# Optimization experiments

Hardware: AMD Instinct MI355X
Metric: run time of the kernel (lower is better)

The kernel has to match this reference:

```python
import jax, jax.numpy as jnp
import numpy as np

GRID, RC, RD, FEAT, HID, PE = 300, 48, 16, 27, 128, 2
B, S = 4096, 128


def _grid_sample(img, grid):
    # img: (G,C,H,W); grid: (G,B,S,2) with (x=width, y=height) in [-1,1]
    # bilinear, align_corners=True (matches torch F.grid_sample defaults used here)
    G, C, H, W = img.shape
    x = (grid[..., 0] + 1.0) * 0.5 * (W - 1)  # (G,B,S)
    y = (grid[..., 1] + 1.0) * 0.5 * (H - 1)
    x0f, y0f = jnp.floor(x), jnp.floor(y)
    x0 = jnp.clip(x0f, 0, W - 1).astype(jnp.int32)
    y0 = jnp.clip(y0f, 0, H - 1).astype(jnp.int32)
    x1 = jnp.clip(x0 + 1, 0, W - 1)
    y1 = jnp.clip(y0 + 1, 0, H - 1)
    wx = (x - x0f)[:, None]  # (G,1,B,S)
    wy = (y - y0f)[:, None]

    def gather(im, yi, xi):  # im (C,H,W), yi/xi (B,S) -> (C,B,S)
        return im[:, yi, xi]

    g = jax.vmap(gather)
    v00 = g(img, y0, x0)
    v01 = g(img, y0, x1)
    v10 = g(img, y1, x0)
    v11 = g(img, y1, x1)
    return (v00 * (1 - wy) * (1 - wx) + v01 * (1 - wy) * wx
            + v10 * wy * (1 - wx) + v11 * wy * wx)  # (G,C,B,S)


def _vm(vectors, matrices, pos):
    # pos: (B,S,3) -> (B,S,3*R)
    b, s = pos.shape[0], pos.shape[1]
    mat_coord = jnp.stack([jnp.stack([pos[..., (i + 1) % 3], pos[..., (i + 2) % 3]], -1)
                           for i in range(3)], 0)  # (3,B,S,2)
    zero = jnp.zeros_like(pos[..., 0])
    vec_coord = jnp.stack([jnp.stack([pos[..., i], zero], -1) for i in range(3)], 0)
    m = _grid_sample(matrices, mat_coord)  # (3,R,B,S)
    v = _grid_sample(vectors, vec_coord)   # (3,R,B,S)
    return (m * v).transpose(2, 3, 0, 1).reshape(b, s, -1)


_COEFFS = (2.0 ** np.linspace(0.0, PE - 1, PE)) * np.pi  # [pi, 2pi]


def _pe(x):
    parts = []
    for c in _COEFFS:
        parts.append(jnp.sin(c * x))
        parts.append(jnp.cos(c * x))
    return jnp.concatenate(parts, -1)


def setup_inputs() -> dict:
    key = jax.random.key(0)
    ks = jax.random.split(key, 12)
    x = jax.random.uniform(ks[0], (B, S, 6), dtype=jnp.float32) * 2.0 - 1.0
    vmc_vec = jax.random.normal(ks[1], (3, RC, GRID, 1), dtype=jnp.float32) * 0.1
    vmc_mat = jax.random.normal(ks[2], (3, RC, GRID, GRID), dtype=jnp.float32) * 0.1
    vmd_vec = jax.random.normal(ks[3], (3, RD, GRID, 1), dtype=jnp.float32) * 0.1
    vmd_mat = jax.random.normal(ks[4], (3, RD, GRID, GRID), dtype=jnp.float32) * 0.1
    feat_w = jax.random.normal(ks[5], (FEAT, 3 * RC), dtype=jnp.float32) / np.sqrt(3 * RC)
    din = (1 + 2 * PE) * (3 + FEAT)  # 150
    w1 = jax.random.normal(ks[6], (HID, din), dtype=jnp.float32) / np.sqrt(din)
    b1 = jnp.zeros((HID,), jnp.float32)
    w2 = jax.random.normal(ks[7], (HID, HID), dtype=jnp.float32) / np.sqrt(HID)
    b2 = jnp.zeros((HID,), jnp.float32)
    w3 = jax.random.normal(ks[8], (3, HID), dtype=jnp.float32) / np.sqrt(HID)
    b3 = jnp.zeros((3,), jnp.float32)
    return {"x": x, "vmc_vec": vmc_vec, "vmc_mat": vmc_mat, "vmd_vec": vmd_vec,
            "vmd_mat": vmd_mat, "feat_w": feat_w, "w1": w1, "b1": b1,
            "w2": w2, "b2": b2, "w3": w3, "b3": b3}


def reference(x, vmc_vec, vmc_mat, vmd_vec, vmd_mat, feat_w, w1, b1, w2, b2, w3, b3):
    pos = x[..., :3]
    dirn = x[..., 3:]
    feature = jnp.einsum('bsk,fk->bsf', _vm(vmc_vec, vmc_mat, pos), feat_w)  # (B,S,27)
    mlp_in = jnp.concatenate([feature, dirn, _pe(feature), _pe(dirn)], -1)  # (B,S,150)
    h = jax.nn.relu(jnp.einsum('bsi,hi->bsh', mlp_in, w1) + b1)
    h = jax.nn.relu(jnp.einsum('bsi,hi->bsh', h, w2) + b2)
    color = jax.nn.sigmoid(jnp.einsum('bsi,oi->bso', h, w3) + b3)  # (B,S,3)
    density = jax.nn.relu(jnp.sum(_vm(vmd_vec, vmd_mat, pos), -1, keepdims=True))
    return jnp.concatenate([color, density], -1)  # (B,S,4)
```

## Files before the change

### kernel.cpp

```cpp
#include <hip/hip_runtime.h>
#include <stdint.h>

typedef unsigned int u32;
typedef _Float16 f16;
typedef __attribute__((ext_vector_type(8))) _Float16 f16x8;
typedef __attribute__((ext_vector_type(4))) float f32x4;
typedef __attribute__((ext_vector_type(2))) float f32x2;

#define XMS 168
#define HS  136

#define WOFF_WEFF 0u
#define WOFF_W1SW 10240u
#define WOFF_W2SW 51200u
#define WOFF_W3SW 83968u
#define WOFF_VD   88064u
#define WOFF_TM   131072u
#define WS_NEED   17411072u

#define TBL_SCALE 64.0f
#define TBL_INV   (1.0f/64.0f)

__global__ void prep_k(const float* __restrict__ feat_w,
                       const float* __restrict__ vmc_vec,
                       const float* __restrict__ vmd_vec,
                       const float* __restrict__ w1,
                       const float* __restrict__ w2,
                       const float* __restrict__ w3,
                       f16* __restrict__ Weff, f16* __restrict__ W1sw,
                       f16* __restrict__ W2sw, f16* __restrict__ W3sw,
                       float* __restrict__ vd)
{
  const int N_WEFF = 5120, N_W1 = 20480, N_W2 = 16384, N_W3 = 2048, N_VD = 48;
  const int total = N_WEFF + N_W1 + N_W2 + N_W3 + N_VD;
  for (int t = blockIdx.x*blockDim.x + threadIdx.x; t < total; t += gridDim.x*blockDim.x){
    if (t < N_WEFF){
      int kb = t >> 10, n = (t >> 5) & 31, kk = t & 31, k = kb*32 + kk;
      float v = 0.f;
      if (n < 27 && k < 144)
        v = feat_w[n*144 + k] * 0.5f*(vmc_vec[k*300+149] + vmc_vec[k*300+150]) * TBL_INV;
      Weff[t] = (f16)v;
    } else if (t < N_WEFF + N_W1){
      int u = t - N_WEFF;
      int kb = u >> 12, n = (u >> 5) & 127, kk = u & 31, k = kb*32 + kk;
      W1sw[u] = (f16)((k < 150) ? w1[n*150 + k] : 0.f);
    } else if (t < N_WEFF + N_W1 + N_W2){
      int u = t - N_WEFF - N_W1;
      int kb = u >> 12, n = (u >> 5) & 127, kk = u & 31, k = kb*32 + kk;
      W2sw[u] = (f16)w2[n*128 + k];
    } else if (t < N_WEFF + N_W1 + N_W2 + N_W3){
      int u = t - N_WEFF - N_W1 - N_W2;
      int kb = u >> 9, n = (u >> 5) & 15, kk = u & 31, k = kb*32 + kk;
      W3sw[u] = (f16)((n < 3) ? w3[n*128 + k] : 0.f);
    } else {
      int k = t - N_WEFF - N_W1 - N_W2 - N_W3;
      vd[k] = 0.5f*(vmd_vec[k*300+149] + vmd_vec[k*300+150]) * TBL_INV;
    }
  }
}

__global__ void pack_feat_k(const float* __restrict__ src, u32* __restrict__ dst)
{
  __shared__ float tile[48*304];
  int i = blockIdx.x / 300, y = blockIdx.x % 300;
  const float* sp = src + (size_t)i*48*90000 + (size_t)y*300;
  for (int t = threadIdx.x; t < 48*300; t += 256){
    int r = t / 300, x = t - r*300;
    tile[r*304 + x] = sp[(size_t)r*90000 + x] * TBL_SCALE;
  }
  __syncthreads();
  u32* dp = dst + (size_t)(i*300 + y)*300*16;
  for (int t = threadIdx.x; t < 300*12; t += 256){
    int x = t / 12, cg = t - x*12;
    int c = cg*4;
    u32 v = __builtin_amdgcn_cvt_pk_fp8_f32(tile[c*304+x],     tile[(c+1)*304+x], 0, false);
    v     = __builtin_amdgcn_cvt_pk_fp8_f32(tile[(c+2)*304+x], tile[(c+3)*304+x], v, true);
    dp[x*16 + cg] = v;
  }
}

__global__ void pack_dens_k(const float* __restrict__ src, u32* __restrict__ dst)
{
  __shared__ float tile[16*304];
  int i = blockIdx.x / 300, y = blockIdx.x % 300;
  const float* sp = src + (size_t)i*16*90000 + (size_t)y*300;
  for (int t = threadIdx.x; t < 16*300; t += 256){
    int r = t / 300, x = t - r*300;
    tile[r*304 + x] = sp[(size_t)r*90000 + x] * TBL_SCALE;
  }
  __syncthreads();
  u32* dp = dst + (size_t)(i*300 + y)*300*16;
  for (int t = threadIdx.x; t < 300*4; t += 256){
    int x = t / 4, cg = t - x*4;
    int c = cg*4;
    u32 v = __builtin_amdgcn_cvt_pk_fp8_f32(tile[c*304+x],     tile[(c+1)*304+x], 0, false);
    v     = __builtin_amdgcn_cvt_pk_fp8_f32(tile[(c+2)*304+x], tile[(c+3)*304+x], v, true);
    dp[x*16 + 12 + cg] = v;
  }
}

__device__ __forceinline__ void decode16(uint4 q, float* o){
  f32x2 t;
  t = __builtin_amdgcn_cvt_pk_f32_fp8(q.x, false); o[0]=t[0];  o[1]=t[1];
  t = __builtin_amdgcn_cvt_pk_f32_fp8(q.x, true ); o[2]=t[0];  o[3]=t[1];
  t = __builtin_amdgcn_cvt_pk_f32_fp8(q.y, false); o[4]=t[0];  o[5]=t[1];
  t = __builtin_amdgcn_cvt_pk_f32_fp8(q.y, true ); o[6]=t[0];  o[7]=t[1];
  t = __builtin_amdgcn_cvt_pk_f32_fp8(q.z, false); o[8]=t[0];  o[9]=t[1];
  t = __builtin_amdgcn_cvt_pk_f32_fp8(q.z, true ); o[10]=t[0]; o[11]=t[1];
  t = __builtin_amdgcn_cvt_pk_f32_fp8(q.w, false); o[12]=t[0]; o[13]=t[1];
  t = __builtin_amdgcn_cvt_pk_f32_fp8(q.w, true ); o[14]=t[0]; o[15]=t[1];
}

__global__ __launch_bounds__(256, 4)
void main_k(const float* __restrict__ xin,
            const f16* __restrict__ WeffSw, const f16* __restrict__ W1sw,
            const f16* __restrict__ W2sw, const f16* __restrict__ W3sw,
            const float* __restrict__ vd,
            const uint4* __restrict__ Tm,
            const float* __restrict__ b1v, const float* __restrict__ b2v,
            const float* __restrict__ b3v, float* __restrict__ out)
{
  __shared__ __align__(16) f16 buf[64*XMS];
  __shared__ __align__(16) f16 bufH[64*HS];
  __shared__ float dLds[192];

  const int tid = threadIdx.x;
  const int l = tid & 63;
  const int w = tid >> 6;
  const size_t nidx = (size_t)blockIdx.x*64 + l;

  const float* xp = xin + nidx*6;
  float p0 = xp[0], p1 = xp[1], p2 = xp[2];

  float dd0=0.f, dd1=0.f, dd2=0.f;
  if (l < 16){
    const float* dp = xin + ((size_t)blockIdx.x*64 + w*16 + l)*6 + 3;
    dd0 = dp[0]; dd1 = dp[1]; dd2 = dp[2];
  }

  if (w < 3){
    float cx = (w==0)? p1 : ((w==1)? p2 : p0);
    float cy = (w==0)? p2 : ((w==1)? p0 : p1);
    float fx = (cx+1.f)*0.5f*299.f, fy = (cy+1.f)*0.5f*299.f;
    float x0f = floorf(fx), y0f = floorf(fy);
    int x0 = min(max((int)x0f,0),299), y0 = min(max((int)y0f,0),299);
    int x1 = min(x0+1,299), y1 = min(y0+1,299);
    float wx = fx-x0f, wy = fy-y0f;
    float w11 = wx*wy, w10 = wy - w11, w01 = wx - w11, w00 = 1.f - wx - wy + w11;

    const uint4* Tb = Tm + (size_t)w*90000*4;
    const uint4* r00 = Tb + (size_t)(y0*300+x0)*4;
    const uint4* r01 = Tb + (size_t)(y0*300+x1)*4;
    const uint4* r10 = Tb + (size_t)(y1*300+x0)*4;
    const uint4* r11 = Tb + (size_t)(y1*300+x1)*4;
    uint4 qa[4], qb[4], qc[4], qd[4];
#pragma unroll
    for (int c4=0;c4<4;++c4){ qa[c4]=r00[c4]; qb[c4]=r01[c4]; qc[c4]=r10[c4]; qd[c4]=r11[c4]; }

    float vdw[16];
#pragma unroll
    for (int j=0;j<16;++j) vdw[j] = vd[w*16 + j];

    f16* dstrow = buf + l*XMS + w*48;
    float dacc = 0.f;
#pragma unroll
    for (int c4=0;c4<4;++c4){
      float A[16],B[16],C[16],D[16];
      decode16(qa[c4],A); decode16(qb[c4],B); decode16(qc[c4],C); decode16(qd[c4],D);
      if (c4 < 3){
        f16x8 o0, o1;
#pragma unroll
        for (int j=0;j<8;++j)
          o0[j] = (f16)(w00*A[j] + w01*B[j] + w10*C[j] + w11*D[j]);
#pragma unroll
        for (int j=0;j<8;++j)
          o1[j] = (f16)(w00*A[8+j] + w01*B[8+j] + w10*C[8+j] + w11*D[8+j]);
        *(f16x8*)(dstrow + c4*16)     = o0;
        *(f16x8*)(dstrow + c4*16 + 8) = o1;
      } else {
#pragma unroll
        for (int j=0;j<16;++j)
          dacc += (w00*A[j] + w01*B[j] + w10*C[j] + w11*D[j]) * vdw[j];
      }
    }
    dLds[w*64 + l] = dacc;
  } else {
    f16x8 z = 0;
    *(f16x8*)(buf + l*XMS + 144) = z;
    *(f16x8*)(buf + l*XMS + 152) = z;
  }
  __syncthreads();

  const int tr = l & 15;
  const int ko = (l >> 4) * 8;

  {
    if (w == 3){
      float ds = dLds[l] + dLds[64 + l] + dLds[128 + l];
      out[nidx*4 + 3] = fmaxf(ds, 0.f);
    }
    f32x4 fa0 = {0.f,0.f,0.f,0.f}, fa1 = {0.f,0.f,0.f,0.f};
    const f16* Arow = buf + (w*16 + tr)*XMS + ko;
#pragma unroll
    for (int kb=0; kb<5; ++kb){
      f16x8 a  = *(const f16x8*)(Arow + kb*32);
      f16x8 b0 = *(const f16x8*)(WeffSw + (size_t)(kb*32 + tr)*32 + ko);
      f16x8 b1 = *(const f16x8*)(WeffSw + (size_t)(kb*32 + 16 + tr)*32 + ko);
      fa0 = __builtin_amdgcn_mfma_f32_16x16x32_f16(a, b0, fa0, 0,0,0);
      fa1 = __builtin_amdgcn_mfma_f32_16x16x32_f16(a, b1, fa1, 0,0,0);
    }
    __builtin_amdgcn_sched_barrier(0);
    asm volatile("" : "+v"(dd0), "+v"(dd1), "+v"(dd2) : "v"(fa0[0]));

    const int sbase = w*16 + (l>>4)*4;
#pragma unroll
    for (int nb=0; nb<2; ++nb){
      int f = nb*16 + tr;
      if (f < 27){
#pragma unroll
        for (int r=0;r<4;++r){
          float fv = nb ? fa1[r] : fa0[r];
          f16* Xr = buf + (sbase + r)*XMS;
          Xr[f] = (f16)fv;
          float a1 = 3.14159265358979f*fv;
          float a2 = 6.28318530717959f*fv;
          Xr[30+f]  = (f16)__sinf(a1);
          Xr[57+f]  = (f16)__cosf(a1);
          Xr[84+f]  = (f16)__sinf(a2);
          Xr[111+f] = (f16)__cosf(a2);
        }
      }
    }
    if (l < 16){
      f16* Xr = buf + (w*16 + l)*XMS;
      Xr[27]=(f16)dd0; Xr[28]=(f16)dd1; Xr[29]=(f16)dd2;
      float dv[3]={dd0,dd1,dd2};
#pragma unroll
      for (int j=0;j<3;++j){
        float a1=3.14159265358979f*dv[j], a2=6.28318530717959f*dv[j];
        Xr[138+j]=(f16)__sinf(a1);
        Xr[141+j]=(f16)__cosf(a1);
        Xr[144+j]=(f16)__sinf(a2);
        Xr[147+j]=(f16)__cosf(a2);
      }
    }
  }
  __syncthreads();

  {
    f32x4 acc[4][2];
#pragma unroll
    for (int m=0;m<4;++m){ acc[m][0]=(f32x4){0.f,0.f,0.f,0.f}; acc[m][1]=(f32x4){0.f,0.f,0.f,0.f}; }
    const int n0 = w*32 + tr;
#pragma unroll
    for (int kb=0; kb<5; ++kb){
      f16x8 b0 = *(const f16x8*)(W1sw + (size_t)(kb*128 + n0)*32 + ko);
      f16x8 b1 = *(const f16x8*)(W1sw + (size_t)(kb*128 + n0 + 16)*32 + ko);
#pragma unroll
      for (int m=0;m<4;++m){
        f16x8 a = *(const f16x8*)(buf + (m*16 + tr)*XMS + kb*32 + ko);
        acc[m][0] = __builtin_amdgcn_mfma_f32_16x16x32_f16(a, b0, acc[m][0], 0,0,0);
        acc[m][1] = __builtin_amdgcn_mfma_f32_16x16x32_f16(a, b1, acc[m][1], 0,0,0);
      }
    }
    float bb0 = b1v[n0], bb1 = b1v[n0+16];
#pragma unroll
    for (int m=0;m<4;++m){
#pragma unroll
      for (int r=0;r<4;++r){
        int ss = m*16 + (l>>4)*4 + r;
        bufH[ss*HS + n0]      = (f16)fmaxf(acc[m][0][r] + bb0, 0.f);
        bufH[ss*HS + n0 + 16] = (f16)fmaxf(acc[m][1][r] + bb1, 0.f);
      }
    }
  }
  __syncthreads();

  {
    f32x4 acc[4][2];
#pragma unroll
    for (int m=0;m<4;++m){ acc[m][0]=(f32x4){0.f,0.f,0.f,0.f}; acc[m][1]=(f32x4){0.f,0.f,0.f,0.f}; }
    const int n0 = w*32 + tr;
#pragma unroll
    for (int kb=0; kb<4; ++kb){
      f16x8 b0 = *(const f16x8*)(W2sw + (size_t)(kb*128 + n0)*32 + ko);
      f16x8 b1 = *(const f16x8*)(W2sw + (size_t)(kb*128 + n0 + 16)*32 + ko);
#pragma unroll
      for (int m=0;m<4;++m){
        f16x8 a = *(const f16x8*)(bufH + (m*16 + tr)*HS + kb*32 + ko);
        acc[m][0] = __builtin_amdgcn_mfma_f32_16x16x32_f16(a, b0, acc[m][0], 0,0,0);
        acc[m][1] = __builtin_amdgcn_mfma_f32_16x16x32_f16(a, b1, acc[m][1], 0,0,0);
      }
    }
    float bb0 = b2v[n0], bb1 = b2v[n0+16];
#pragma unroll
    for (int m=0;m<4;++m){
#pragma unroll
      for (int r=0;r<4;++r){
        int ss = m*16 + (l>>4)*4 + r;
        buf[ss*HS + n0]      = (f16)fmaxf(acc[m][0][r] + bb0, 0.f);
        buf[ss*HS + n0 + 16] = (f16)fmaxf(acc[m][1][r] + bb1, 0.f);
      }
    }
  }
  __syncthreads();

  {
    f32x4 acc = {0.f,0.f,0.f,0.f};
#pragma unroll
    for (int kb=0; kb<4; ++kb){
      f16x8 a = *(const f16x8*)(buf + (w*16 + tr)*HS + kb*32 + ko);
      f16x8 b = *(const f16x8*)(W3sw + (size_t)(kb*16 + tr)*32 + ko);
      acc = __builtin_amdgcn_mfma_f32_16x16x32_f16(a, b, acc, 0,0,0);
    }
    if (tr < 3){
      float bb = b3v[tr];
#pragma unroll
      for (int r=0;r<4;++r){
        int ss = w*16 + (l>>4)*4 + r;
        float c = acc[r] + bb;
        out[((size_t)blockIdx.x*64 + ss)*4 + tr] = 1.f/(1.f + __expf(-c));
      }
    }
  }
}

extern "C" void kernel_launch(void* const* d_in, const int* in_sizes, int n_in,
                              void* d_out, int out_size, void* d_ws, size_t ws_size,
                              hipStream_t stream)
{
  const float* xin     = (const float*)d_in[0];
  const float* vmc_vec = (const float*)d_in[1];
  const float* vmc_mat = (const float*)d_in[2];
  const float* vmd_vec = (const float*)d_in[3];
  const float* vmd_mat = (const float*)d_in[4];
  const float* feat_w  = (const float*)d_in[5];
  const float* w1      = (const float*)d_in[6];
  const float* b1      = (const float*)d_in[7];
  const float* w2      = (const float*)d_in[8];
  const float* b2      = (const float*)d_in[9];
  const float* w3      = (const float*)d_in[10];
  const float* b3      = (const float*)d_in[11];
  float* out = (float*)d_out;

  char* ws = (char*)d_ws;
  f16*   Weff = (f16*)(ws + WOFF_WEFF);
  f16*   W1sw = (f16*)(ws + WOFF_W1SW);
  f16*   W2sw = (f16*)(ws + WOFF_W2SW);
  f16*   W3sw = (f16*)(ws + WOFF_W3SW);
  float* vd   = (float*)(ws + WOFF_VD);
  u32*   Tm   = (u32*)(ws + WOFF_TM);

  prep_k<<<64, 256, 0, stream>>>(feat_w, vmc_vec, vmd_vec, w1, w2, w3,
                                 Weff, W1sw, W2sw, W3sw, vd);
  pack_feat_k<<<900, 256, 0, stream>>>(vmc_mat, Tm);
  pack_dens_k<<<900, 256, 0, stream>>>(vmd_mat, Tm);

  main_k<<<8192, 256, 0, stream>>>(xin, Weff, W1sw, W2sw, W3sw, vd,
                                   (const uint4*)Tm, b1, b2, b3, out);
}
```

Baseline: 183.7 us.

## Split fused kernel into gather and MLP kernels via workspace staging buffer

Splits the fused sample-plus-MLP kernel into two kernels: a gather kernel that does the table sampling and feature projection and writes the 160-wide f16 MLP input rows to a workspace buffer, and an MLP kernel that reads them back and runs the three layers. The split is taken only when the workspace is large enough, with the old fused kernel kept as a fallback. The aim is to let the latency-bound gather phase run at higher occupancy, with its own launch bounds and less shared memory, separate from the MFMA-heavy MLP. The cost is an extra global round trip of about 168 MB of intermediates and one more kernel launch.

```diff
diff --git a/kernel.cpp b/kernel.cpp
--- a/kernel.cpp
+++ b/kernel.cpp
@@ -16,6 +16,8 @@
 #define WOFF_W3SW 83968u
 #define WOFF_VD   88064u
 #define WOFF_TM   131072u
+#define WOFF_XG   17411072u
+#define WS_SPLIT  185183232u
 #define WS_NEED   17411072u
 
 #define TBL_SCALE 64.0f
@@ -111,30 +113,18 @@
   t = __builtin_amdgcn_cvt_pk_f32_fp8(q.w, true ); o[14]=t[0]; o[15]=t[1];
 }
 
-__global__ __launch_bounds__(256, 4)
-void main_k(const float* __restrict__ xin,
-            const f16* __restrict__ WeffSw, const f16* __restrict__ W1sw,
-            const f16* __restrict__ W2sw, const f16* __restrict__ W3sw,
-            const float* __restrict__ vd,
-            const uint4* __restrict__ Tm,
-            const float* __restrict__ b1v, const float* __restrict__ b2v,
-            const float* __restrict__ b3v, float* __restrict__ out)
-{
-  __shared__ __align__(16) f16 buf[64*XMS];
-  __shared__ __align__(16) f16 bufH[64*HS];
-  __shared__ float dLds[192];
-
-  const int tid = threadIdx.x;
-  const int l = tid & 63;
-  const int w = tid >> 6;
-  const size_t nidx = (size_t)blockIdx.x*64 + l;
-
+__device__ __forceinline__ void sample_and_fold(
+    const float* __restrict__ xin, const f16* __restrict__ WeffSw,
+    const float* __restrict__ vd, const uint4* __restrict__ Tm,
+    float* __restrict__ out, f16* buf, float* dLds,
+    int tid, int l, int w, size_t nidx)
+{
   const float* xp = xin + nidx*6;
   float p0 = xp[0], p1 = xp[1], p2 = xp[2];
 
   float dd0=0.f, dd1=0.f, dd2=0.f;
   if (l < 16){
-    const float* dp = xin + ((size_t)blockIdx.x*64 + w*16 + l)*6 + 3;
+    const float* dp = xin + (nidx - l + w*16 + l)*6 + 3;
     dd0 = dp[0]; dd1 = dp[1]; dd2 = dp[2];
   }
 
@@ -194,58 +184,104 @@
   const int tr = l & 15;
   const int ko = (l >> 4) * 8;
 
-  {
-    if (w == 3){
-      float ds = dLds[l] + dLds[64 + l] + dLds[128 + l];
-      out[nidx*4 + 3] = fmaxf(ds, 0.f);
-    }
-    f32x4 fa0 = {0.f,0.f,0.f,0.f}, fa1 = {0.f,0.f,0.f,0.f};
-    const f16* Arow = buf + (w*16 + tr)*XMS + ko;
-#pragma unroll
-    for (int kb=0; kb<5; ++kb){
-      f16x8 a  = *(const f16x8*)(Arow + kb*32);
-      f16x8 b0 = *(const f16x8*)(WeffSw + (size_t)(kb*32 + tr)*32 + ko);
-      f16x8 b1 = *(const f16x8*)(WeffSw + (size_t)(kb*32 + 16 + tr)*32 + ko);
-      fa0 = __builtin_amdgcn_mfma_f32_16x16x32_f16(a, b0, fa0, 0,0,0);
-      fa1 = __builtin_amdgcn_mfma_f32_16x16x32_f16(a, b1, fa1, 0,0,0);
-    }
-    __builtin_amdgcn_sched_barrier(0);
-    asm volatile("" : "+v"(dd0), "+v"(dd1), "+v"(dd2) : "v"(fa0[0]));
-
-    const int sbase = w*16 + (l>>4)*4;
-#pragma unroll
-    for (int nb=0; nb<2; ++nb){
-      int f = nb*16 + tr;
-      if (f < 27){
-#pragma unroll
-        for (int r=0;r<4;++r){
-          float fv = nb ? fa1[r] : fa0[r];
-          f16* Xr = buf + (sbase + r)*XMS;
-          Xr[f] = (f16)fv;
-          float a1 = 3.14159265358979f*fv;
-          float a2 = 6.28318530717959f*fv;
-          Xr[30+f]  = (f16)__sinf(a1);
-          Xr[57+f]  = (f16)__cosf(a1);
-          Xr[84+f]  = (f16)__sinf(a2);
-          Xr[111+f] = (f16)__cosf(a2);
-        }
-      }
-    }
-    if (l < 16){
-      f16* Xr = buf + (w*16 + l)*XMS;
-      Xr[27]=(f16)dd0; Xr[28]=(f16)dd1; Xr[29]=(f16)dd2;
-      float dv[3]={dd0,dd1,dd2};
-#pragma unroll
-      for (int j=0;j<3;++j){
-        float a1=3.14159265358979f*dv[j], a2=6.28318530717959f*dv[j];
-        Xr[138+j]=(f16)__sinf(a1);
-        Xr[141+j]=(f16)__cosf(a1);
-        Xr[144+j]=(f16)__sinf(a2);
-        Xr[147+j]=(f16)__cosf(a2);
-      }
-    }
-  }
-  __syncthreads();
+  if (w == 3){
+    float ds = dLds[l] + dLds[64 + l] + dLds[128 + l];
+    out[nidx*4 + 3] = fmaxf(ds, 0.f);
+  }
+  f32x4 fa0 = {0.f,0.f,0.f,0.f}, fa1 = {0.f,0.f,0.f,0.f};
+  const f16* Arow = buf + (w*16 + tr)*XMS + ko;
+#pragma unroll
+  for (int kb=0; kb<5; ++kb){
+    f16x8 a  = *(const f16x8*)(Arow + kb*32);
+    f16x8 b0 = *(const f16x8*)(WeffSw + (size_t)(kb*32 + tr)*32 + ko);
+    f16x8 b1 = *(const f16x8*)(WeffSw + (size_t)(kb*32 + 16 + tr)*32 + ko);
+    fa0 = __builtin_amdgcn_mfma_f32_16x16x32_f16(a, b0, fa0, 0,0,0);
+    fa1 = __builtin_amdgcn_mfma_f32_16x16x32_f16(a, b1, fa1, 0,0,0);
+  }
+  __builtin_amdgcn_sched_barrier(0);
+  asm volatile("" : "+v"(dd0), "+v"(dd1), "+v"(dd2) : "v"(fa0[0]));
+
+  const int sbase = w*16 + (l>>4)*4;
+#pragma unroll
+  for (int nb=0; nb<2; ++nb){
+    int f = nb*16 + tr;
+    if (f < 27){
+#pragma unroll
+      for (int r=0;r<4;++r){
+        float fv = nb ? fa1[r] : fa0[r];
+        f16* Xr = buf + (sbase + r)*XMS;
+        Xr[f] = (f16)fv;
+        float a1 = 3.14159265358979f*fv;
+        float a2 = 6.28318530717959f*fv;
+        Xr[30+f]  = (f16)__sinf(a1);
+        Xr[57+f]  = (f16)__cosf(a1);
+        Xr[84+f]  = (f16)__sinf(a2);
+        Xr[111+f] = (f16)__cosf(a2);
+      }
+    }
+  }
+  if (l < 16){
+    f16* Xr = buf + (w*16 + l)*XMS;
+    Xr[27]=(f16)dd0; Xr[28]=(f16)dd1; Xr[29]=(f16)dd2;
+    float dv[3]={dd0,dd1,dd2};
+#pragma unroll
+    for (int j=0;j<3;++j){
+      float a1=3.14159265358979f*dv[j], a2=6.28318530717959f*dv[j];
+      Xr[138+j]=(f16)__sinf(a1);
+      Xr[141+j]=(f16)__cosf(a1);
+      Xr[144+j]=(f16)__sinf(a2);
+      Xr[147+j]=(f16)__cosf(a2);
+    }
+  }
+}
+
+__global__ __launch_bounds__(256, 6)
+void gather_k(const float* __restrict__ xin,
+              const f16* __restrict__ WeffSw, const float* __restrict__ vd,
+              const uint4* __restrict__ Tm, f16* __restrict__ Xg,
+              float* __restrict__ out)
+{
+  __shared__ __align__(16) f16 buf[64*XMS];
+  __shared__ float dLds[192];
+  const int tid = threadIdx.x;
+  const int l = tid & 63, w = tid >> 6;
+  const size_t nidx = (size_t)blockIdx.x*64 + l;
+
+  sample_and_fold(xin, WeffSw, vd, Tm, out, buf, dLds, tid, l, w, nidx);
+  __syncthreads();
+
+  f16* dst = Xg + (size_t)blockIdx.x*64*160;
+#pragma unroll
+  for (int it=0; it<5; ++it){
+    int i = tid + it*256;
+    int row = i / 20, q = i - row*20;
+    *(f16x8*)(dst + row*160 + q*8) = *(const f16x8*)(buf + row*XMS + q*8);
+  }
+}
+
+__global__ __launch_bounds__(256, 4)
+void mlp_k(const f16* __restrict__ Xg,
+           const f16* __restrict__ W1sw, const f16* __restrict__ W2sw,
+           const f16* __restrict__ W3sw,
+           const float* __restrict__ b1v, const float* __restrict__ b2v,
+           const float* __restrict__ b3v, float* __restrict__ out)
+{
+  __shared__ __align__(16) f16 buf[64*XMS];
+  __shared__ __align__(16) f16 bufH[64*HS];
+  const int tid = threadIdx.x;
+  const int l = tid & 63, w = tid >> 6;
+
+  const f16* src = Xg + (size_t)blockIdx.x*64*160;
+#pragma unroll
+  for (int it=0; it<5; ++it){
+    int i = tid + it*256;
+    int row = i / 20, q = i - row*20;
+    *(f16x8*)(buf + row*XMS + q*8) = *(const f16x8*)(src + row*160 + q*8);
+  }
+  __syncthreads();
+
+  const int tr = l & 15;
+  const int ko = (l >> 4) * 8;
 
   {
     f32x4 acc[4][2];
@@ -305,6 +341,105 @@
   }
   __syncthreads();
 
+  {
+    f32x4 acc = {0.f,0.f,0.f,0.f};
+#pragma unroll
+    for (int kb=0; kb<4; ++kb){
+      f16x8 a = *(const f16x8*)(buf + (w*16 + tr)*HS + kb*32 + ko);
+      f16x8 b = *(const f16x8*)(W3sw + (size_t)(kb*16 + tr)*32 + ko);
+      acc = __builtin_amdgcn_mfma_f32_16x16x32_f16(a, b, acc, 0,0,0);
+    }
+    if (tr < 3){
+      float bb = b3v[tr];
+#pragma unroll
+      for (int r=0;r<4;++r){
+        int ss = w*16 + (l>>4)*4 + r;
+        float c = acc[r] + bb;
+        out[((size_t)blockIdx.x*64 + ss)*4 + tr] = 1.f/(1.f + __expf(-c));
+      }
+    }
+  }
+}
+
+__global__ __launch_bounds__(256, 4)
+void main_k(const float* __restrict__ xin,
+            const f16* __restrict__ WeffSw, const f16* __restrict__ W1sw,
+            const f16* __restrict__ W2sw, const f16* __restrict__ W3sw,
+            const float* __restrict__ vd,
+            const uint4* __restrict__ Tm,
+            const float* __restrict__ b1v, const float* __restrict__ b2v,
+            const float* __restrict__ b3v, float* __restrict__ out)
+{
+  __shared__ __align__(16) f16 buf[64*XMS];
+  __shared__ __align__(16) f16 bufH[64*HS];
+  __shared__ float dLds[192];
+
+  const int tid = threadIdx.x;
+  const int l = tid & 63, w = tid >> 6;
+  const size_t nidx = (size_t)blockIdx.x*64 + l;
+
+  sample_and_fold(xin, WeffSw, vd, Tm, out, buf, dLds, tid, l, w, nidx);
+  __syncthreads();
+
+  const int tr = l & 15;
+  const int ko = (l >> 4) * 8;
+
+  {
+    f32x4 acc[4][2];
+#pragma unroll
+    for (int m=0;m<4;++m){ acc[m][0]=(f32x4){0.f,0.f,0.f,0.f}; acc[m][1]=(f32x4){0.f,0.f,0.f,0.f}; }
+    const int n0 = w*32 + tr;
+#pragma unroll
+    for (int kb=0; kb<5; ++kb){
+      f16x8 b0 = *(const f16x8*)(W1sw + (size_t)(kb*128 + n0)*32 + ko);
+      f16x8 b1 = *(const f16x8*)(W1sw + (size_t)(kb*128 + n0 + 16)*32 + ko);
+#pragma unroll
+      for (int m=0;m<4;++m){
+        f16x8 a = *(const f16x8*)(buf + (m*16 + tr)*XMS + kb*32 + ko);
+        acc[m][0] = __builtin_amdgcn_mfma_f32_16x16x32_f16(a, b0, acc[m][0], 0,0,0);
+        acc[m][1] = __builtin_amdgcn_mfma_f32_16x16x32_f16(a, b1, acc[m][1], 0,0,0);
+      }
+    }
+    float bb0 = b1v[n0], bb1 = b1v[n0+16];
+#pragma unroll
+    for (int m=0;m<4;++m){
+#pragma unroll
+      for (int r=0;r<4;++r){
+        int ss = m*16 + (l>>4)*4 + r;
+        bufH[ss*HS + n0]      = (f16)fmaxf(acc[m][0][r] + bb0, 0.f);
+        bufH[ss*HS + n0 + 16] = (f16)fmaxf(acc[m][1][r] + bb1, 0.f);
+      }
+    }
+  }
+  __syncthreads();
+  {
+    f32x4 acc[4][2];
+#pragma unroll
+    for (int m=0;m<4;++m){ acc[m][0]=(f32x4){0.f,0.f,0.f,0.f}; acc[m][1]=(f32x4){0.f,0.f,0.f,0.f}; }
+    const int n0 = w*32 + tr;
+#pragma unroll
+    for (int kb=0; kb<4; ++kb){
+      f16x8 b0 = *(const f16x8*)(W2sw + (size_t)(kb*128 + n0)*32 + ko);
+      f16x8 b1 = *(const f16x8*)(W2sw + (size_t)(kb*128 + n0 + 16)*32 + ko);
+#pragma unroll
+      for (int m=0;m<4;++m){
+        f16x8 a = *(const f16x8*)(bufH + (m*16 + tr)*HS + kb*32 + ko);
+        acc[m][0] = __builtin_amdgcn_mfma_f32_16x16x32_f16(a, b0, acc[m][0], 0,0,0);
+        acc[m][1] = __builtin_amdgcn_mfma_f32_16x16x32_f16(a, b1, acc[m][1], 0,0,0);
+      }
+    }
+    float bb0 = b2v[n0], bb1 = b2v[n0+16];
+#pragma unroll
+    for (int m=0;m<4;++m){
+#pragma unroll
+      for (int r=0;r<4;++r){
+        int ss = m*16 + (l>>4)*4 + r;
+        buf[ss*HS + n0]      = (f16)fmaxf(acc[m][0][r] + bb0, 0.f);
+        buf[ss*HS + n0 + 16] = (f16)fmaxf(acc[m][1][r] + bb1, 0.f);
+      }
+    }
+  }
+  __syncthreads();
   {
     f32x4 acc = {0.f,0.f,0.f,0.f};
 #pragma unroll
@@ -350,12 +485,18 @@
   f16*   W3sw = (f16*)(ws + WOFF_W3SW);
   float* vd   = (float*)(ws + WOFF_VD);
   u32*   Tm   = (u32*)(ws + WOFF_TM);
+  f16*   Xg   = (f16*)(ws + WOFF_XG);
 
   prep_k<<<64, 256, 0, stream>>>(feat_w, vmc_vec, vmd_vec, w1, w2, w3,
                                  Weff, W1sw, W2sw, W3sw, vd);
   pack_feat_k<<<900, 256, 0, stream>>>(vmc_mat, Tm);
   pack_dens_k<<<900, 256, 0, stream>>>(vmd_mat, Tm);
 
-  main_k<<<8192, 256, 0, stream>>>(xin, Weff, W1sw, W2sw, W3sw, vd,
-                                   (const uint4*)Tm, b1, b2, b3, out);
-}
+  if (ws_size >= (size_t)WS_SPLIT){
+    gather_k<<<8192, 256, 0, stream>>>(xin, Weff, vd, (const uint4*)Tm, Xg, out);
+    mlp_k<<<8192, 256, 0, stream>>>(Xg, W1sw, W2sw, W3sw, b1, b2, b3, out);
+  } else {
+    main_k<<<8192, 256, 0, stream>>>(xin, Weff, W1sw, W2sw, W3sw, vd,
+                                     (const uint4*)Tm, b1, b2, b3, out);
+  }
+}
```

After: 388.9 us. +111.7%, slower.

## Sort samples by Morton cell before gather to improve table-access locality

Applied to the files above, without the earlier changes.

Adds a counting sort of the 524288 samples by a 15-bit Morton key of their position (histogram, single-block scan, atomic scatter). The main kernel then reads the sorted inputs, with tiles interleaved across blocks, and writes outputs through the permutation. The aim is better cache locality for the random bilinear gathers into the 17 MB fp8 table. The cost is four extra launches, a serial scan and extra global traffic. The two pack kernels are also merged into one launch.

```diff
diff --git a/kernel.cpp b/kernel.cpp
--- a/kernel.cpp
+++ b/kernel.cpp
@@ -9,6 +9,9 @@
 
 #define XMS 168
 #define HS  136
+
+#define NS   524288
+#define NBIN 32768
 
 #define WOFF_WEFF 0u
 #define WOFF_W1SW 10240u
@@ -16,7 +19,12 @@
 #define WOFF_W3SW 83968u
 #define WOFF_VD   88064u
 #define WOFF_TM   131072u
-#define WS_NEED   17411072u
+#define WOFF_HIST 17411072u
+#define WOFF_CUR  17542144u
+#define WOFF_KEYS 17673216u
+#define WOFF_PERM 19770368u
+#define WOFF_XS   21867520u
+#define WS_NEED   34450432u
 
 #define TBL_SCALE 64.0f
 #define TBL_INV   (1.0f/64.0f)
@@ -59,19 +67,25 @@
   }
 }
 
-__global__ void pack_feat_k(const float* __restrict__ src, u32* __restrict__ dst)
+__global__ void pack_k(const float* __restrict__ feat, const float* __restrict__ dens,
+                       u32* __restrict__ dst)
 {
   __shared__ float tile[48*304];
-  int i = blockIdx.x / 300, y = blockIdx.x % 300;
-  const float* sp = src + (size_t)i*48*90000 + (size_t)y*300;
-  for (int t = threadIdx.x; t < 48*300; t += 256){
+  int b = blockIdx.x;
+  bool isf = b < 900;
+  int bb = isf ? b : b - 900;
+  int i = bb / 300, y = bb % 300;
+  int C = isf ? 48 : 16;
+  const float* sp = (isf ? feat : dens) + (size_t)i*C*90000 + (size_t)y*300;
+  for (int t = threadIdx.x; t < C*300; t += 256){
     int r = t / 300, x = t - r*300;
     tile[r*304 + x] = sp[(size_t)r*90000 + x] * TBL_SCALE;
   }
   __syncthreads();
-  u32* dp = dst + (size_t)(i*300 + y)*300*16;
-  for (int t = threadIdx.x; t < 300*12; t += 256){
-    int x = t / 12, cg = t - x*12;
+  u32* dp = dst + (size_t)(i*300 + y)*300*16 + (isf ? 0 : 12);
+  int ng = C >> 2;
+  for (int t = threadIdx.x; t < 300*ng; t += 256){
+    int x = t / ng, cg = t - x*ng;
     int c = cg*4;
     u32 v = __builtin_amdgcn_cvt_pk_fp8_f32(tile[c*304+x],     tile[(c+1)*304+x], 0, false);
     v     = __builtin_amdgcn_cvt_pk_fp8_f32(tile[(c+2)*304+x], tile[(c+3)*304+x], v, true);
@@ -79,24 +93,65 @@
   }
 }
 
-__global__ void pack_dens_k(const float* __restrict__ src, u32* __restrict__ dst)
-{
-  __shared__ float tile[16*304];
-  int i = blockIdx.x / 300, y = blockIdx.x % 300;
-  const float* sp = src + (size_t)i*16*90000 + (size_t)y*300;
-  for (int t = threadIdx.x; t < 16*300; t += 256){
-    int r = t / 300, x = t - r*300;
-    tile[r*304 + x] = sp[(size_t)r*90000 + x] * TBL_SCALE;
-  }
-  __syncthreads();
-  u32* dp = dst + (size_t)(i*300 + y)*300*16;
-  for (int t = threadIdx.x; t < 300*4; t += 256){
-    int x = t / 4, cg = t - x*4;
-    int c = cg*4;
-    u32 v = __builtin_amdgcn_cvt_pk_fp8_f32(tile[c*304+x],     tile[(c+1)*304+x], 0, false);
-    v     = __builtin_amdgcn_cvt_pk_fp8_f32(tile[(c+2)*304+x], tile[(c+3)*304+x], v, true);
-    dp[x*16 + 12 + cg] = v;
-  }
+__global__ void zero_k(u32* __restrict__ h){ h[blockIdx.x*1024 + threadIdx.x] = 0u; }
+
+__device__ __forceinline__ u32 mcell(float p){
+  int c = (int)((p + 1.f)*16.f);
+  return (u32)min(31, max(0, c));
+}
+__device__ __forceinline__ u32 morton15(u32 a, u32 b, u32 c){
+  u32 r = 0;
+#pragma unroll
+  for (int i=0;i<5;++i)
+    r |= (((a>>i)&1u)<<(3*i+2)) | (((b>>i)&1u)<<(3*i+1)) | (((c>>i)&1u)<<(3*i));
+  return r;
+}
+
+__global__ void key_k(const float* __restrict__ xin, u32* __restrict__ keys,
+                      u32* __restrict__ hist)
+{
+  int t = blockIdx.x*256 + threadIdx.x;
+  const float* xp = xin + (size_t)t*6;
+  u32 k = morton15(mcell(xp[0]), mcell(xp[1]), mcell(xp[2]));
+  keys[t] = k;
+  atomicAdd(&hist[k], 1u);
+}
+
+__global__ __launch_bounds__(1024, 1)
+void scan_k(const u32* __restrict__ hist, u32* __restrict__ cur)
+{
+  __shared__ u32 s[1024];
+  int t = threadIdx.x;
+  u32 loc[32];
+  u32 sum = 0;
+  const u32* hp = hist + t*32;
+#pragma unroll
+  for (int j=0;j<32;++j){ loc[j] = sum; sum += hp[j]; }
+  s[t] = sum;
+  __syncthreads();
+  for (int off=1; off<1024; off<<=1){
+    u32 v = (t >= off) ? s[t-off] : 0u;
+    __syncthreads();
+    s[t] += v;
+    __syncthreads();
+  }
+  u32 base = (t == 0) ? 0u : s[t-1];
+  u32* cp = cur + t*32;
+#pragma unroll
+  for (int j=0;j<32;++j) cp[j] = base + loc[j];
+}
+
+__global__ void scatter_k(const float* __restrict__ xin, const u32* __restrict__ keys,
+                          u32* __restrict__ cur, u32* __restrict__ perm,
+                          float* __restrict__ xs)
+{
+  int t = blockIdx.x*256 + threadIdx.x;
+  u32 k = keys[t];
+  u32 pos = atomicAdd(&cur[k], 1u);
+  perm[pos] = (u32)t;
+  const float* sp = xin + (size_t)t*6;
+  float* dp = xs + (size_t)pos*6;
+  dp[0]=sp[0]; dp[1]=sp[1]; dp[2]=sp[2]; dp[3]=sp[3]; dp[4]=sp[4]; dp[5]=sp[5];
 }
 
 __device__ __forceinline__ void decode16(uint4 q, float* o){
@@ -111,8 +166,9 @@
   t = __builtin_amdgcn_cvt_pk_f32_fp8(q.w, true ); o[14]=t[0]; o[15]=t[1];
 }
 
+template<bool SORTED>
 __global__ __launch_bounds__(256, 4)
-void main_k(const float* __restrict__ xin,
+void main_k(const float* __restrict__ xs, const u32* __restrict__ perm,
             const f16* __restrict__ WeffSw, const f16* __restrict__ W1sw,
             const f16* __restrict__ W2sw, const f16* __restrict__ W3sw,
             const float* __restrict__ vd,
@@ -127,14 +183,23 @@
   const int tid = threadIdx.x;
   const int l = tid & 63;
   const int w = tid >> 6;
-  const size_t nidx = (size_t)blockIdx.x*64 + l;
-
-  const float* xp = xin + nidx*6;
+
+  const int tile = SORTED ? ((blockIdx.x & 7)*1024 + (blockIdx.x >> 3)) : blockIdx.x;
+  const size_t base = (size_t)tile*64;
+
+  const float* xp = xs + (base + l)*6;
   float p0 = xp[0], p1 = xp[1], p2 = xp[2];
+
+  u32 pmL = SORTED ? perm[base + l] : (u32)(base + l);
+  const int ssb = w*16 + (l>>4)*4;
+  u32 pmr[4];
+#pragma unroll
+  for (int r=0;r<4;++r)
+    pmr[r] = SORTED ? perm[base + ssb + r] : (u32)(base + ssb + r);
 
   float dd0=0.f, dd1=0.f, dd2=0.f;
   if (l < 16){
-    const float* dp = xin + ((size_t)blockIdx.x*64 + w*16 + l)*6 + 3;
+    const float* dp = xs + (base + w*16 + l)*6 + 3;
     dd0 = dp[0]; dd1 = dp[1]; dd2 = dp[2];
   }
 
@@ -197,7 +262,7 @@
   {
     if (w == 3){
       float ds = dLds[l] + dLds[64 + l] + dLds[128 + l];
-      out[nidx*4 + 3] = fmaxf(ds, 0.f);
+      out[(size_t)pmL*4 + 3] = fmaxf(ds, 0.f);
     }
     f32x4 fa0 = {0.f,0.f,0.f,0.f}, fa1 = {0.f,0.f,0.f,0.f};
     const f16* Arow = buf + (w*16 + tr)*XMS + ko;
@@ -212,7 +277,7 @@
     __builtin_amdgcn_sched_barrier(0);
     asm volatile("" : "+v"(dd0), "+v"(dd1), "+v"(dd2) : "v"(fa0[0]));
 
-    const int sbase = w*16 + (l>>4)*4;
+    const int sbase = ssb;
 #pragma unroll
     for (int nb=0; nb<2; ++nb){
       int f = nb*16 + tr;
@@ -317,9 +382,8 @@
       float bb = b3v[tr];
 #pragma unroll
       for (int r=0;r<4;++r){
-        int ss = w*16 + (l>>4)*4 + r;
         float c = acc[r] + bb;
-        out[((size_t)blockIdx.x*64 + ss)*4 + tr] = 1.f/(1.f + __expf(-c));
+        out[(size_t)pmr[r]*4 + tr] = 1.f/(1.f + __expf(-c));
       }
     }
   }
@@ -350,12 +414,25 @@
   f16*   W3sw = (f16*)(ws + WOFF_W3SW);
   float* vd   = (float*)(ws + WOFF_VD);
   u32*   Tm   = (u32*)(ws + WOFF_TM);
+  u32*   hist = (u32*)(ws + WOFF_HIST);
+  u32*   cur  = (u32*)(ws + WOFF_CUR);
+  u32*   keys = (u32*)(ws + WOFF_KEYS);
+  u32*   perm = (u32*)(ws + WOFF_PERM);
+  float* xs   = (float*)(ws + WOFF_XS);
 
   prep_k<<<64, 256, 0, stream>>>(feat_w, vmc_vec, vmd_vec, w1, w2, w3,
                                  Weff, W1sw, W2sw, W3sw, vd);
-  pack_feat_k<<<900, 256, 0, stream>>>(vmc_mat, Tm);
-  pack_dens_k<<<900, 256, 0, stream>>>(vmd_mat, Tm);
-
-  main_k<<<8192, 256, 0, stream>>>(xin, Weff, W1sw, W2sw, W3sw, vd,
-                                   (const uint4*)Tm, b1, b2, b3, out);
-}
+  pack_k<<<1800, 256, 0, stream>>>(vmc_mat, vmd_mat, Tm);
+
+  if (ws_size >= (size_t)WS_NEED){
+    zero_k<<<32, 1024, 0, stream>>>(hist);
+    key_k<<<2048, 256, 0, stream>>>(xin, keys, hist);
+    scan_k<<<1, 1024, 0, stream>>>(hist, cur);
+    scatter_k<<<2048, 256, 0, stream>>>(xin, keys, cur, perm, xs);
+    main_k<true><<<8192, 256, 0, stream>>>(xs, perm, Weff, W1sw, W2sw, W3sw, vd,
+                                           (const uint4*)Tm, b1, b2, b3, out);
+  } else {
+    main_k<false><<<8192, 256, 0, stream>>>(xin, nullptr, Weff, W1sw, W2sw, W3sw, vd,
+                                            (const uint4*)Tm, b1, b2, b3, out);
+  }
+}
```

Measured after the change: 230.6 us. 1.26x slower.

## Process two 64-sample tiles per block and overlap corner gathers with MLP

Applied to the files above, without the earlier changes.

The main kernel now handles 128 samples per block in two halves. The table-corner gathers for the second half are issued before the first half's MLP runs, so their memory latency can hide behind MFMA work. The MLP loops are also reordered per m-tile to cut live accumulator registers, and the two pack kernels are merged into one launch. The gathered corner data stays live across the MLP, which raises register pressure, and halving the grid reduces the number of blocks available to fill the GPU.

```diff
diff --git a/kernel.cpp b/kernel.cpp
--- a/kernel.cpp
+++ b/kernel.cpp
@@ -59,43 +59,29 @@
   }
 }
 
-__global__ void pack_feat_k(const float* __restrict__ src, u32* __restrict__ dst)
+__global__ void pack_k(const float* __restrict__ feat, const float* __restrict__ dens,
+                       u32* __restrict__ dst)
 {
   __shared__ float tile[48*304];
-  int i = blockIdx.x / 300, y = blockIdx.x % 300;
-  const float* sp = src + (size_t)i*48*90000 + (size_t)y*300;
-  for (int t = threadIdx.x; t < 48*300; t += 256){
+  int b = blockIdx.x;
+  bool isf = b < 900;
+  int bb = isf ? b : b - 900;
+  int i = bb / 300, y = bb % 300;
+  int C = isf ? 48 : 16;
+  const float* sp = (isf ? feat : dens) + (size_t)i*C*90000 + (size_t)y*300;
+  for (int t = threadIdx.x; t < C*300; t += 256){
     int r = t / 300, x = t - r*300;
     tile[r*304 + x] = sp[(size_t)r*90000 + x] * TBL_SCALE;
   }
   __syncthreads();
-  u32* dp = dst + (size_t)(i*300 + y)*300*16;
-  for (int t = threadIdx.x; t < 300*12; t += 256){
-    int x = t / 12, cg = t - x*12;
+  u32* dp = dst + (size_t)(i*300 + y)*300*16 + (isf ? 0 : 12);
+  int ng = C >> 2;
+  for (int t = threadIdx.x; t < 300*ng; t += 256){
+    int x = t / ng, cg = t - x*ng;
     int c = cg*4;
     u32 v = __builtin_amdgcn_cvt_pk_fp8_f32(tile[c*304+x],     tile[(c+1)*304+x], 0, false);
     v     = __builtin_amdgcn_cvt_pk_fp8_f32(tile[(c+2)*304+x], tile[(c+3)*304+x], v, true);
     dp[x*16 + cg] = v;
-  }
-}
-
-__global__ void pack_dens_k(const float* __restrict__ src, u32* __restrict__ dst)
-{
-  __shared__ float tile[16*304];
-  int i = blockIdx.x / 300, y = blockIdx.x % 300;
-  const float* sp = src + (size_t)i*16*90000 + (size_t)y*300;
-  for (int t = threadIdx.x; t < 16*300; t += 256){
-    int r = t / 300, x = t - r*300;
-    tile[r*304 + x] = sp[(size_t)r*90000 + x] * TBL_SCALE;
-  }
-  __syncthreads();
-  u32* dp = dst + (size_t)(i*300 + y)*300*16;
-  for (int t = threadIdx.x; t < 300*4; t += 256){
-    int x = t / 4, cg = t - x*4;
-    int c = cg*4;
-    u32 v = __builtin_amdgcn_cvt_pk_fp8_f32(tile[c*304+x],     tile[(c+1)*304+x], 0, false);
-    v     = __builtin_amdgcn_cvt_pk_fp8_f32(tile[(c+2)*304+x], tile[(c+3)*304+x], v, true);
-    dp[x*16 + 12 + cg] = v;
   }
 }
 
@@ -127,77 +113,85 @@
   const int tid = threadIdx.x;
   const int l = tid & 63;
   const int w = tid >> 6;
-  const size_t nidx = (size_t)blockIdx.x*64 + l;
-
-  const float* xp = xin + nidx*6;
-  float p0 = xp[0], p1 = xp[1], p2 = xp[2];
-
-  float dd0=0.f, dd1=0.f, dd2=0.f;
-  if (l < 16){
-    const float* dp = xin + ((size_t)blockIdx.x*64 + w*16 + l)*6 + 3;
-    dd0 = dp[0]; dd1 = dp[1]; dd2 = dp[2];
-  }
-
-  if (w < 3){
-    float cx = (w==0)? p1 : ((w==1)? p2 : p0);
-    float cy = (w==0)? p2 : ((w==1)? p0 : p1);
-    float fx = (cx+1.f)*0.5f*299.f, fy = (cy+1.f)*0.5f*299.f;
-    float x0f = floorf(fx), y0f = floorf(fy);
-    int x0 = min(max((int)x0f,0),299), y0 = min(max((int)y0f,0),299);
-    int x1 = min(x0+1,299), y1 = min(y0+1,299);
-    float wx = fx-x0f, wy = fy-y0f;
-    float w11 = wx*wy, w10 = wy - w11, w01 = wx - w11, w00 = 1.f - wx - wy + w11;
-
-    const uint4* Tb = Tm + (size_t)w*90000*4;
-    const uint4* r00 = Tb + (size_t)(y0*300+x0)*4;
-    const uint4* r01 = Tb + (size_t)(y0*300+x1)*4;
-    const uint4* r10 = Tb + (size_t)(y1*300+x0)*4;
-    const uint4* r11 = Tb + (size_t)(y1*300+x1)*4;
-    uint4 qa[4], qb[4], qc[4], qd[4];
-#pragma unroll
-    for (int c4=0;c4<4;++c4){ qa[c4]=r00[c4]; qb[c4]=r01[c4]; qc[c4]=r10[c4]; qd[c4]=r11[c4]; }
-
-    float vdw[16];
-#pragma unroll
-    for (int j=0;j<16;++j) vdw[j] = vd[w*16 + j];
-
-    f16* dstrow = buf + l*XMS + w*48;
-    float dacc = 0.f;
-#pragma unroll
-    for (int c4=0;c4<4;++c4){
-      float A[16],B[16],C[16],D[16];
-      decode16(qa[c4],A); decode16(qb[c4],B); decode16(qc[c4],C); decode16(qd[c4],D);
-      if (c4 < 3){
-        f16x8 o0, o1;
-#pragma unroll
-        for (int j=0;j<8;++j)
-          o0[j] = (f16)(w00*A[j] + w01*B[j] + w10*C[j] + w11*D[j]);
-#pragma unroll
-        for (int j=0;j<8;++j)
-          o1[j] = (f16)(w00*A[8+j] + w01*B[8+j] + w10*C[8+j] + w11*D[8+j]);
-        *(f16x8*)(dstrow + c4*16)     = o0;
-        *(f16x8*)(dstrow + c4*16 + 8) = o1;
-      } else {
-#pragma unroll
-        for (int j=0;j<16;++j)
-          dacc += (w00*A[j] + w01*B[j] + w10*C[j] + w11*D[j]) * vdw[j];
-      }
-    }
-    dLds[w*64 + l] = dacc;
-  } else {
-    f16x8 z = 0;
-    *(f16x8*)(buf + l*XMS + 144) = z;
-    *(f16x8*)(buf + l*XMS + 152) = z;
-  }
-  __syncthreads();
-
   const int tr = l & 15;
   const int ko = (l >> 4) * 8;
-
-  {
+  const int rbase = w*16 + (l>>4)*4;
+
+  const size_t base0 = (size_t)blockIdx.x * 128;
+  const size_t base1 = base0 + 64;
+
+  uint4 qa[4], qb[4], qc[4], qd[4];
+  float w00=0.f, w01=0.f, w10=0.f, w11=0.f;
+
+  auto load_pos = [&](size_t base, float& PX, float& PY, float& PZ,
+                      float& D0, float& D1, float& D2){
+    const float* xp = xin + (base + l)*6;
+    PX = xp[0]; PY = xp[1]; PZ = xp[2];
+    if (l < 16){
+      const float* dp = xin + (base + w*16 + l)*6 + 3;
+      D0 = dp[0]; D1 = dp[1]; D2 = dp[2];
+    }
+  };
+
+  auto issue_corners = [&](float PX, float PY, float PZ){
+    if (w < 3){
+      float cx = (w==0)? PY : ((w==1)? PZ : PX);
+      float cy = (w==0)? PZ : ((w==1)? PX : PY);
+      float fx = (cx+1.f)*0.5f*299.f, fy = (cy+1.f)*0.5f*299.f;
+      float x0f = floorf(fx), y0f = floorf(fy);
+      int x0 = min(max((int)x0f,0),299), y0 = min(max((int)y0f,0),299);
+      int x1 = min(x0+1,299), y1 = min(y0+1,299);
+      float wx = fx-x0f, wy = fy-y0f;
+      w11 = wx*wy; w10 = wy - w11; w01 = wx - w11; w00 = 1.f - wx - wy + w11;
+      const uint4* Tb = Tm + (size_t)w*90000*4;
+      const uint4* r00 = Tb + (size_t)(y0*300+x0)*4;
+      const uint4* r01 = Tb + (size_t)(y0*300+x1)*4;
+      const uint4* r10 = Tb + (size_t)(y1*300+x0)*4;
+      const uint4* r11 = Tb + (size_t)(y1*300+x1)*4;
+#pragma unroll
+      for (int c4=0;c4<4;++c4){ qa[c4]=r00[c4]; qb[c4]=r01[c4]; qc[c4]=r10[c4]; qd[c4]=r11[c4]; }
+    }
+  };
+
+  auto lerp_store = [&](){
+    if (w < 3){
+      float vdw[16];
+#pragma unroll
+      for (int j=0;j<16;++j) vdw[j] = vd[w*16 + j];
+      f16* dstrow = buf + l*XMS + w*48;
+      float dacc = 0.f;
+#pragma unroll
+      for (int c4=0;c4<4;++c4){
+        float A[16],B[16],C[16],D[16];
+        decode16(qa[c4],A); decode16(qb[c4],B); decode16(qc[c4],C); decode16(qd[c4],D);
+        if (c4 < 3){
+          f16x8 o0, o1;
+#pragma unroll
+          for (int j=0;j<8;++j)
+            o0[j] = (f16)(w00*A[j] + w01*B[j] + w10*C[j] + w11*D[j]);
+#pragma unroll
+          for (int j=0;j<8;++j)
+            o1[j] = (f16)(w00*A[8+j] + w01*B[8+j] + w10*C[8+j] + w11*D[8+j]);
+          *(f16x8*)(dstrow + c4*16)     = o0;
+          *(f16x8*)(dstrow + c4*16 + 8) = o1;
+        } else {
+#pragma unroll
+          for (int j=0;j<16;++j)
+            dacc += (w00*A[j] + w01*B[j] + w10*C[j] + w11*D[j]) * vdw[j];
+        }
+      }
+      dLds[w*64 + l] = dacc;
+    } else {
+      f16x8 z = 0;
+      *(f16x8*)(buf + l*XMS + 144) = z;
+      *(f16x8*)(buf + l*XMS + 152) = z;
+    }
+  };
+
+  auto fold_pe = [&](size_t base, float D0, float D1, float D2){
     if (w == 3){
       float ds = dLds[l] + dLds[64 + l] + dLds[128 + l];
-      out[nidx*4 + 3] = fmaxf(ds, 0.f);
+      out[(base + l)*4 + 3] = fmaxf(ds, 0.f);
     }
     f32x4 fa0 = {0.f,0.f,0.f,0.f}, fa1 = {0.f,0.f,0.f,0.f};
     const f16* Arow = buf + (w*16 + tr)*XMS + ko;
@@ -210,9 +204,8 @@
       fa1 = __builtin_amdgcn_mfma_f32_16x16x32_f16(a, b1, fa1, 0,0,0);
     }
     __builtin_amdgcn_sched_barrier(0);
-    asm volatile("" : "+v"(dd0), "+v"(dd1), "+v"(dd2) : "v"(fa0[0]));
-
-    const int sbase = w*16 + (l>>4)*4;
+    asm volatile("" : "+v"(D0), "+v"(D1), "+v"(D2) : "v"(fa0[0]));
+
 #pragma unroll
     for (int nb=0; nb<2; ++nb){
       int f = nb*16 + tr;
@@ -220,7 +213,7 @@
 #pragma unroll
         for (int r=0;r<4;++r){
           float fv = nb ? fa1[r] : fa0[r];
-          f16* Xr = buf + (sbase + r)*XMS;
+          f16* Xr = buf + (rbase + r)*XMS;
           Xr[f] = (f16)fv;
           float a1 = 3.14159265358979f*fv;
           float a2 = 6.28318530717959f*fv;
@@ -233,8 +226,8 @@
     }
     if (l < 16){
       f16* Xr = buf + (w*16 + l)*XMS;
-      Xr[27]=(f16)dd0; Xr[28]=(f16)dd1; Xr[29]=(f16)dd2;
-      float dv[3]={dd0,dd1,dd2};
+      Xr[27]=(f16)D0; Xr[28]=(f16)D1; Xr[29]=(f16)D2;
+      float dv[3]={D0,D1,D2};
 #pragma unroll
       for (int j=0;j<3;++j){
         float a1=3.14159265358979f*dv[j], a2=6.28318530717959f*dv[j];
@@ -244,85 +237,87 @@
         Xr[147+j]=(f16)__cosf(a2);
       }
     }
-  }
-  __syncthreads();
-
-  {
-    f32x4 acc[4][2];
-#pragma unroll
-    for (int m=0;m<4;++m){ acc[m][0]=(f32x4){0.f,0.f,0.f,0.f}; acc[m][1]=(f32x4){0.f,0.f,0.f,0.f}; }
+  };
+
+  auto mlp = [&](size_t base){
     const int n0 = w*32 + tr;
 #pragma unroll
-    for (int kb=0; kb<5; ++kb){
-      f16x8 b0 = *(const f16x8*)(W1sw + (size_t)(kb*128 + n0)*32 + ko);
-      f16x8 b1 = *(const f16x8*)(W1sw + (size_t)(kb*128 + n0 + 16)*32 + ko);
-#pragma unroll
-      for (int m=0;m<4;++m){
-        f16x8 a = *(const f16x8*)(buf + (m*16 + tr)*XMS + kb*32 + ko);
-        acc[m][0] = __builtin_amdgcn_mfma_f32_16x16x32_f16(a, b0, acc[m][0], 0,0,0);
-        acc[m][1] = __builtin_amdgcn_mfma_f32_16x16x32_f16(a, b1, acc[m][1], 0,0,0);
-      }
-    }
-    float bb0 = b1v[n0], bb1 = b1v[n0+16];
-#pragma unroll
-    for (int m=0;m<4;++m){
+    for (int m=0; m<4; ++m){
+      f32x4 a0 = {0.f,0.f,0.f,0.f}, a1v = {0.f,0.f,0.f,0.f};
+#pragma unroll
+      for (int kb=0; kb<5; ++kb){
+        f16x8 b0 = *(const f16x8*)(W1sw + (size_t)(kb*128 + n0)*32 + ko);
+        f16x8 b1 = *(const f16x8*)(W1sw + (size_t)(kb*128 + n0 + 16)*32 + ko);
+        f16x8 a  = *(const f16x8*)(buf + (m*16 + tr)*XMS + kb*32 + ko);
+        a0  = __builtin_amdgcn_mfma_f32_16x16x32_f16(a, b0, a0, 0,0,0);
+        a1v = __builtin_amdgcn_mfma_f32_16x16x32_f16(a, b1, a1v, 0,0,0);
+      }
+      float bb0 = b1v[n0], bb1 = b1v[n0+16];
 #pragma unroll
       for (int r=0;r<4;++r){
         int ss = m*16 + (l>>4)*4 + r;
-        bufH[ss*HS + n0]      = (f16)fmaxf(acc[m][0][r] + bb0, 0.f);
-        bufH[ss*HS + n0 + 16] = (f16)fmaxf(acc[m][1][r] + bb1, 0.f);
-      }
-    }
-  }
-  __syncthreads();
-
-  {
-    f32x4 acc[4][2];
-#pragma unroll
-    for (int m=0;m<4;++m){ acc[m][0]=(f32x4){0.f,0.f,0.f,0.f}; acc[m][1]=(f32x4){0.f,0.f,0.f,0.f}; }
-    const int n0 = w*32 + tr;
-#pragma unroll
-    for (int kb=0; kb<4; ++kb){
-      f16x8 b0 = *(const f16x8*)(W2sw + (size_t)(kb*128 + n0)*32 + ko);
-      f16x8 b1 = *(const f16x8*)(W2sw + (size_t)(kb*128 + n0 + 16)*32 + ko);
-#pragma unroll
-      for (int m=0;m<4;++m){
-        f16x8 a = *(const f16x8*)(bufH + (m*16 + tr)*HS + kb*32 + ko);
-        acc[m][0] = __builtin_amdgcn_mfma_f32_16x16x32_f16(a, b0, acc[m][0], 0,0,0);
-        acc[m][1] = __builtin_amdgcn_mfma_f32_16x16x32_f16(a, b1, acc[m][1], 0,0,0);
-      }
-    }
-    float bb0 = b2v[n0], bb1 = b2v[n0+16];
-#pragma unroll
-    for (int m=0;m<4;++m){
+        bufH[ss*HS + n0]      = (f16)fmaxf(a0[r] + bb0, 0.f);
+        bufH[ss*HS + n0 + 16] = (f16)fmaxf(a1v[r] + bb1, 0.f);
+      }
+    }
+    __syncthreads();
+#pragma unroll
+    for (int m=0; m<4; ++m){
+      f32x4 a0 = {0.f,0.f,0.f,0.f}, a1v = {0.f,0.f,0.f,0.f};
+#pragma unroll
+      for (int kb=0; kb<4; ++kb){
+        f16x8 b0 = *(const f16x8*)(W2sw + (size_t)(kb*128 + n0)*32 + ko);
+        f16x8 b1 = *(const f16x8*)(W2sw + (size_t)(kb*128 + n0 + 16)*32 + ko);
+        f16x8 a  = *(const f16x8*)(bufH + (m*16 + tr)*HS + kb*32 + ko);
+        a0  = __builtin_amdgcn_mfma_f32_16x16x32_f16(a, b0, a0, 0,0,0);
+        a1v = __builtin_amdgcn_mfma_f32_16x16x32_f16(a, b1, a1v, 0,0,0);
+      }
+      float bb0 = b2v[n0], bb1 = b2v[n0+16];
 #pragma unroll
       for (int r=0;r<4;++r){
         int ss = m*16 + (l>>4)*4 + r;
-        buf[ss*HS + n0]      = (f16)fmaxf(acc[m][0][r] + bb0, 0.f);
-        buf[ss*HS + n0 + 16] = (f16)fmaxf(acc[m][1][r] + bb1, 0.f);
-      }
-    }
-  }
-  __syncthreads();
-
-  {
-    f32x4 acc = {0.f,0.f,0.f,0.f};
-#pragma unroll
-    for (int kb=0; kb<4; ++kb){
-      f16x8 a = *(const f16x8*)(buf + (w*16 + tr)*HS + kb*32 + ko);
-      f16x8 b = *(const f16x8*)(W3sw + (size_t)(kb*16 + tr)*32 + ko);
-      acc = __builtin_amdgcn_mfma_f32_16x16x32_f16(a, b, acc, 0,0,0);
-    }
-    if (tr < 3){
-      float bb = b3v[tr];
-#pragma unroll
-      for (int r=0;r<4;++r){
-        int ss = w*16 + (l>>4)*4 + r;
-        float c = acc[r] + bb;
-        out[((size_t)blockIdx.x*64 + ss)*4 + tr] = 1.f/(1.f + __expf(-c));
-      }
-    }
-  }
+        buf[ss*HS + n0]      = (f16)fmaxf(a0[r] + bb0, 0.f);
+        buf[ss*HS + n0 + 16] = (f16)fmaxf(a1v[r] + bb1, 0.f);
+      }
+    }
+    __syncthreads();
+    {
+      f32x4 acc = {0.f,0.f,0.f,0.f};
+#pragma unroll
+      for (int kb=0; kb<4; ++kb){
+        f16x8 a = *(const f16x8*)(buf + (w*16 + tr)*HS + kb*32 + ko);
+        f16x8 b = *(const f16x8*)(W3sw + (size_t)(kb*16 + tr)*32 + ko);
+        acc = __builtin_amdgcn_mfma_f32_16x16x32_f16(a, b, acc, 0,0,0);
+      }
+      if (tr < 3){
+        float bb = b3v[tr];
+#pragma unroll
+        for (int r=0;r<4;++r){
+          float c = acc[r] + bb;
+          out[(base + rbase + r)*4 + tr] = 1.f/(1.f + __expf(-c));
+        }
+      }
+    }
+  };
+
+  float px0,py0,pz0, e00=0.f,e01=0.f,e02=0.f;
+  float px1,py1,pz1, e10=0.f,e11=0.f,e12=0.f;
+
+  load_pos(base0, px0,py0,pz0, e00,e01,e02);
+  issue_corners(px0,py0,pz0);
+  lerp_store();
+  __syncthreads();
+  load_pos(base1, px1,py1,pz1, e10,e11,e12);
+  fold_pe(base0, e00,e01,e02);
+  __syncthreads();
+  issue_corners(px1,py1,pz1);
+  mlp(base0);
+  __syncthreads();
+  lerp_store();
+  __syncthreads();
+  fold_pe(base1, e10,e11,e12);
+  __syncthreads();
+  mlp(base1);
 }
 
 extern "C" void kernel_launch(void* const* d_in, const int* in_sizes, int n_in,
@@ -353,9 +348,8 @@
 
   prep_k<<<64, 256, 0, stream>>>(feat_w, vmc_vec, vmd_vec, w1, w2, w3,
                                  Weff, W1sw, W2sw, W3sw, vd);
-  pack_feat_k<<<900, 256, 0, stream>>>(vmc_mat, Tm);
-  pack_dens_k<<<900, 256, 0, stream>>>(vmd_mat, Tm);
-
-  main_k<<<8192, 256, 0, stream>>>(xin, Weff, W1sw, W2sw, W3sw, vd,
+  pack_k<<<1800, 256, 0, stream>>>(vmc_mat, vmd_mat, Tm);
+
+  main_k<<<4096, 256, 0, stream>>>(xin, Weff, W1sw, W2sw, W3sw, vd,
                                    (const uint4*)Tm, b1, b2, b3, out);
 }
```

After: 268.1 us. 45.9% more time.
